# Optimization experiments

Measured on AMD Instinct MI355X. Metric: run time of the kernel, lower is better.

Reference implementation:

```python
import jax, jax.numpy as jnp
import numpy as np

N_NODES = 100000
N_EDGES = 1600000
D_FEAT = 32
D_HID = 64
D_OUT = 64


def setup_inputs() -> dict:
    key = jax.random.key(0)
    ks = jax.random.split(key, 7)
    x = jax.random.normal(ks[0], (N_NODES, D_FEAT), dtype=jnp.float32)
    pos = jax.random.uniform(ks[1], (N_NODES, 3), dtype=jnp.float32) * 100.0
    # Fixed-size stand-in for radius_graph(pos, 5) output: (2, E) [source; target]
    edge_index = jax.random.randint(ks[2], (2, N_EDGES), 0, N_NODES, dtype=jnp.int64)
    d_in = D_FEAT + 3  # concat(x_j, pos_j - pos_i)
    W1 = jax.random.normal(ks[3], (d_in, D_HID), dtype=jnp.float32) / np.sqrt(d_in)
    b1 = jnp.zeros((D_HID,), dtype=jnp.float32)
    W2 = jax.random.normal(ks[4], (D_HID, D_OUT), dtype=jnp.float32) / np.sqrt(D_HID)
    b2 = jnp.zeros((D_OUT,), dtype=jnp.float32)
    return {"x": x, "pos": pos, "edge_index": edge_index,
            "W1": W1, "b1": b1, "W2": W2, "b2": b2}


def reference(x, pos, edge_index, W1, b1, W2, b2):
    n = x.shape[0]
    # PointNetConv default add_self_loops=True (radius_graph used loop=False)
    loops = jnp.arange(n, dtype=edge_index.dtype)
    src = jnp.concatenate([edge_index[0], loops])  # source j
    dst = jnp.concatenate([edge_index[1], loops])  # target i
    # gather: per-edge message input [E+N, d_feat+3]
    msg_in = jnp.concatenate([x[src], pos[src] - pos[dst]], axis=-1)
    # local_nn MLP
    h = jax.nn.relu(msg_in @ W1 + b1) @ W2 + b2
    # scatter: max-aggregate onto target nodes (PointConv aggr='max')
    out = jax.ops.segment_max(h, dst, num_segments=n)
    return out
```

## Files before the change

### kernel.cpp

```cpp
#include <hip/hip_runtime.h>
#include <math.h>

#define N_NODES 100000
#define N_EDGES 1600000
#define D_FEAT 32
#define D_HID 64
#define D_OUT 64
#define CAP 48
#define NPB 64
#define NBKT 1563
#define B1 256
#define E_PER_B1 6250
#define NB_NODE 1024

typedef _Float16 half8 __attribute__((ext_vector_type(8)));
typedef float f32x4  __attribute__((ext_vector_type(4)));

__device__ inline unsigned pk_subrelu(unsigned v, unsigned nq) {
    unsigned r;
    asm("v_pk_add_f16 %0, %1, %2\n\t"
        "v_pk_max_f16 %0, %0, 0"
        : "=v"(r) : "v"(v), "v"(nq));
    return r;
}

__global__ __launch_bounds__(256)
void node_kernel(const float* __restrict__ x,
                 const float* __restrict__ pos,
                 const float* __restrict__ W1,
                 const float* __restrict__ b1,
                 unsigned short* __restrict__ vb,
                 unsigned short* __restrict__ qb) {
    const int lane = threadIdx.x & 63;
    const int wid  = (blockIdx.x * blockDim.x + threadIdx.x) >> 6;
    const int nw   = (NB_NODE * 256) >> 6;

    float w[D_FEAT + 3];
#pragma unroll
    for (int f = 0; f < D_FEAT + 3; ++f)
        w[f] = W1[f * D_HID + lane];
    const float bb = b1[lane];

    for (int node = wid; node < N_NODES; node += nw) {
        const float* xr = x + (size_t)node * D_FEAT;
        float acc = bb;
#pragma unroll
        for (int f = 0; f < D_FEAT; ++f)
            acc = fmaf(xr[f], w[f], acc);

        const float* pr = pos + (size_t)node * 3;
        float qa = 0.0f;
#pragma unroll
        for (int p = 0; p < 3; ++p)
            qa = fmaf(pr[p], w[D_FEAT + p], qa);

        vb[(size_t)node * D_HID + lane] =
            __builtin_bit_cast(unsigned short, (_Float16)(acc + qa));
        qb[(size_t)node * D_HID + lane] =
            __builtin_bit_cast(unsigned short, (_Float16)(-qa));
    }
}

__global__ __launch_bounds__(1024)
void sort_kernel(const int* __restrict__ src,
                 const int* __restrict__ dst,
                 unsigned int* __restrict__ coarse,
                 int* __restrict__ dir) {
    __shared__ int hist[NBKT];
    __shared__ int stage[E_PER_B1];
    __shared__ int wsum[16];

    const int tid  = threadIdx.x;
    const int lane = tid & 63;
    const int wv   = tid >> 6;
    const int e0   = blockIdx.x * E_PER_B1;

    for (int b = tid; b < NBKT; b += 1024) hist[b] = 0;
    __syncthreads();

    for (int e = e0 + tid; e < e0 + E_PER_B1; e += 1024)
        atomicAdd(&hist[dst[e] >> 6], 1);
    __syncthreads();

    const int i0 = tid * 2;
    int c0 = (i0     < NBKT) ? hist[i0]     : 0;
    int c1 = (i0 + 1 < NBKT) ? hist[i0 + 1] : 0;
    const int sum = c0 + c1;
    int inc = sum;
#pragma unroll
    for (int d = 1; d < 64; d <<= 1) {
        int u = __shfl_up(inc, d, 64);
        if (lane >= d) inc += u;
    }
    if (lane == 63) wsum[wv] = inc;
    __syncthreads();
    if (wv == 0) {
        int s = (lane < 16) ? wsum[lane] : 0;
#pragma unroll
        for (int d = 1; d < 16; d <<= 1) {
            int u = __shfl_up(s, d, 64);
            if (lane >= d) s += u;
        }
        if (lane < 16) wsum[lane] = s;
    }
    __syncthreads();
    const int excl = inc - sum + ((wv > 0) ? wsum[wv - 1] : 0);
    if (i0     < NBKT) hist[i0]     = excl;
    if (i0 + 1 < NBKT) hist[i0 + 1] = excl + c0;
    __syncthreads();

    for (int b = tid; b < NBKT; b += 1024)
        dir[(size_t)blockIdx.x * NBKT + b] = e0 + hist[b];
    __syncthreads();

    for (int e = e0 + tid; e < e0 + E_PER_B1; e += 1024) {
        int d = dst[e], s = src[e];
        int p = atomicAdd(&hist[d >> 6], 1);
        stage[p] = (int)(((unsigned)s << 6) | (unsigned)(d & 63));
    }
    __syncthreads();

    for (int i = tid; i < E_PER_B1; i += 1024)
        coarse[e0 + i] = (unsigned)stage[i];
}

__global__ __launch_bounds__(256)
void agg_kernel(const unsigned short* __restrict__ vb,
                const unsigned short* __restrict__ qb,
                const float* __restrict__ W2,
                const float* __restrict__ b2,
                const int* __restrict__ dir,
                const unsigned int* __restrict__ coarse,
                float* __restrict__ out) {
    __shared__ int lcnt[NPB];
    __shared__ int lslots[NPB][CAP];

    const int tid  = threadIdx.x;
    const int lane = tid & 63;
    const int wave = tid >> 6;
    const int quad = lane >> 4;
    const int mrow = lane & 15;
    const int bkt  = blockIdx.x;
    const int nbase = bkt << 6;

    half8 bfrag[4][2];
#pragma unroll
    for (int t = 0; t < 4; ++t)
#pragma unroll
        for (int kh = 0; kh < 2; ++kh) {
            half8 f;
#pragma unroll
            for (int j = 0; j < 8; ++j)
                f[j] = (_Float16)W2[(kh * 32 + quad * 8 + j) * D_OUT + t * 16 + mrow];
            bfrag[t][kh] = f;
        }
    float bias[4];
#pragma unroll
    for (int t = 0; t < 4; ++t) bias[t] = b2[t * 16 + mrow];

    for (int i = tid; i < NPB; i += 256) lcnt[i] = 0;
    __syncthreads();
    {
        const int s0 = dir[(size_t)tid * NBKT + bkt];
        const int s1 = (bkt + 1 < NBKT) ? dir[(size_t)tid * NBKT + bkt + 1]
                                        : (tid + 1) * E_PER_B1;
        for (int j = s0; j < s1; ++j) {
            unsigned enc = coarse[j];
            int local = (int)(enc & 63u);
            int s     = (int)(enc >> 6);
            int p = atomicAdd(&lcnt[local], 1);
            if (p < CAP) lslots[local][p] = s;
        }
    }
    __syncthreads();

    for (int ln = wave; ln < NPB; ln += 4) {
        const int node = nbase + ln;
        if (node >= N_NODES) break;

        const uint4 nq0 = *(const uint4*)(qb + (size_t)node * D_HID + quad * 8);
        const uint4 nq1 = *(const uint4*)(qb + (size_t)node * D_HID + 32 + quad * 8);

        int deg = lcnt[ln];
        if (deg > CAP) deg = CAP;
        const int rows = deg + 1;
        const int nbat = (rows + 15) >> 4;

        float rmax[4][4];
#pragma unroll
        for (int t = 0; t < 4; ++t)
#pragma unroll
            for (int r = 0; r < 4; ++r) rmax[t][r] = -INFINITY;

        for (int b = 0; b < nbat; ++b) {
            int idx = b * 16 + mrow;
            int idxc = (idx < CAP) ? idx : (CAP - 1);
            int s = (idx < deg) ? lslots[ln][idxc] : node;

            const uint4 v0 = *(const uint4*)(vb + (size_t)s * D_HID + quad * 8);
            const uint4 v1 = *(const uint4*)(vb + (size_t)s * D_HID + 32 + quad * 8);

            uint4 a0u, a1u;
            a0u.x = pk_subrelu(v0.x, nq0.x);
            a0u.y = pk_subrelu(v0.y, nq0.y);
            a0u.z = pk_subrelu(v0.z, nq0.z);
            a0u.w = pk_subrelu(v0.w, nq0.w);
            a1u.x = pk_subrelu(v1.x, nq1.x);
            a1u.y = pk_subrelu(v1.y, nq1.y);
            a1u.z = pk_subrelu(v1.z, nq1.z);
            a1u.w = pk_subrelu(v1.w, nq1.w);
            half8 a0 = __builtin_bit_cast(half8, a0u);
            half8 a1 = __builtin_bit_cast(half8, a1u);

#pragma unroll
            for (int t = 0; t < 4; ++t) {
                f32x4 acc = (f32x4){0.f, 0.f, 0.f, 0.f};
                acc = __builtin_amdgcn_mfma_f32_16x16x32_f16(a0, bfrag[t][0], acc, 0, 0, 0);
                acc = __builtin_amdgcn_mfma_f32_16x16x32_f16(a1, bfrag[t][1], acc, 0, 0, 0);
#pragma unroll
                for (int r = 0; r < 4; ++r)
                    rmax[t][r] = fmaxf(rmax[t][r], acc[r]);
            }
        }

        float fin[4];
#pragma unroll
        for (int t = 0; t < 4; ++t) {
            float m = fmaxf(fmaxf(rmax[t][0], rmax[t][1]), fmaxf(rmax[t][2], rmax[t][3]));
            m = fmaxf(m, __shfl_xor(m, 16, 64));
            m = fmaxf(m, __shfl_xor(m, 32, 64));
            fin[t] = m + bias[t];
        }
        float r = (quad == 0) ? fin[0] : (quad == 1) ? fin[1] : (quad == 2) ? fin[2] : fin[3];
        out[(size_t)node * D_OUT + lane] = r;
    }
}

extern "C" void kernel_launch(void* const* d_in, const int* in_sizes, int n_in,
                              void* d_out, int out_size, void* d_ws, size_t ws_size,
                              hipStream_t stream) {
    const float* x   = (const float*)d_in[0];
    const float* pos = (const float*)d_in[1];
    const int*   ei  = (const int*)d_in[2];
    const float* W1  = (const float*)d_in[3];
    const float* b1  = (const float*)d_in[4];
    const float* W2  = (const float*)d_in[5];
    const float* b2  = (const float*)d_in[6];
    float* out = (float*)d_out;

    char* ws = (char*)d_ws;
    unsigned short* vb   = (unsigned short*)ws;
    unsigned short* qb   = (unsigned short*)(ws + 12800000);
    unsigned int* coarse = (unsigned int*)(ws + 25600000);
    int*            dir  = (int*)(ws + 32000000);

    const int* src = ei;
    const int* dst = ei + N_EDGES;

    hipLaunchKernelGGL(sort_kernel, dim3(B1), dim3(1024), 0, stream,
                       src, dst, coarse, dir);
    hipLaunchKernelGGL(node_kernel, dim3(NB_NODE), dim3(256), 0, stream,
                       x, pos, W1, b1, vb, qb);
    hipLaunchKernelGGL(agg_kernel, dim3(NBKT), dim3(256), 0, stream,
                       vb, qb, W2, b2, dir, coarse, out);
}
```

Before: 194.1 us.

## Halve nodes per aggregation bucket and transpose bucket directory layout

Buckets shrink from 64 to 32 destination nodes, doubling the number of aggregation blocks to spread work across more CUs. The sort kernel scans four histogram entries per thread to cover the larger bucket count. The per-block bucket offsets are now stored bucket-major, so each aggregation block reads its 256 start offsets contiguously instead of with a large stride. Each block keeps four waves but now handles only 32 nodes, so per-block setup such as the W2 fragment load is amortised over fewer nodes. The node-bound check is dropped because 3125*32 equals the node count exactly.

```diff
diff --git a/kernel.cpp b/kernel.cpp
--- a/kernel.cpp
+++ b/kernel.cpp
@@ -7,8 +7,8 @@
 #define D_HID 64
 #define D_OUT 64
 #define CAP 48
-#define NPB 64
-#define NBKT 1563
+#define NPB 32
+#define NBKT 3125
 #define B1 256
 #define E_PER_B1 6250
 #define NB_NODE 1024
@@ -65,7 +65,7 @@
 void sort_kernel(const int* __restrict__ src,
                  const int* __restrict__ dst,
                  unsigned int* __restrict__ coarse,
-                 int* __restrict__ dir) {
+                 int* __restrict__ dirT) {
     __shared__ int hist[NBKT];
     __shared__ int stage[E_PER_B1];
     __shared__ int wsum[16];
@@ -79,13 +79,17 @@
     __syncthreads();
 
     for (int e = e0 + tid; e < e0 + E_PER_B1; e += 1024)
-        atomicAdd(&hist[dst[e] >> 6], 1);
-    __syncthreads();
-
-    const int i0 = tid * 2;
-    int c0 = (i0     < NBKT) ? hist[i0]     : 0;
-    int c1 = (i0 + 1 < NBKT) ? hist[i0 + 1] : 0;
-    const int sum = c0 + c1;
+        atomicAdd(&hist[dst[e] >> 5], 1);
+    __syncthreads();
+
+    const int i0 = tid * 4;
+    int c[4];
+    int sum = 0;
+#pragma unroll
+    for (int k = 0; k < 4; ++k) {
+        c[k] = (i0 + k < NBKT) ? hist[i0 + k] : 0;
+        sum += c[k];
+    }
     int inc = sum;
 #pragma unroll
     for (int d = 1; d < 64; d <<= 1) {
@@ -104,19 +108,22 @@
         if (lane < 16) wsum[lane] = s;
     }
     __syncthreads();
-    const int excl = inc - sum + ((wv > 0) ? wsum[wv - 1] : 0);
-    if (i0     < NBKT) hist[i0]     = excl;
-    if (i0 + 1 < NBKT) hist[i0 + 1] = excl + c0;
+    int excl = inc - sum + ((wv > 0) ? wsum[wv - 1] : 0);
+#pragma unroll
+    for (int k = 0; k < 4; ++k) {
+        if (i0 + k < NBKT) hist[i0 + k] = excl;
+        excl += c[k];
+    }
     __syncthreads();
 
     for (int b = tid; b < NBKT; b += 1024)
-        dir[(size_t)blockIdx.x * NBKT + b] = e0 + hist[b];
+        dirT[(size_t)b * B1 + blockIdx.x] = e0 + hist[b];
     __syncthreads();
 
     for (int e = e0 + tid; e < e0 + E_PER_B1; e += 1024) {
         int d = dst[e], s = src[e];
-        int p = atomicAdd(&hist[d >> 6], 1);
-        stage[p] = (int)(((unsigned)s << 6) | (unsigned)(d & 63));
+        int p = atomicAdd(&hist[d >> 5], 1);
+        stage[p] = (int)(((unsigned)s << 5) | (unsigned)(d & 31));
     }
     __syncthreads();
 
@@ -129,7 +136,7 @@
                 const unsigned short* __restrict__ qb,
                 const float* __restrict__ W2,
                 const float* __restrict__ b2,
-                const int* __restrict__ dir,
+                const int* __restrict__ dirT,
                 const unsigned int* __restrict__ coarse,
                 float* __restrict__ out) {
     __shared__ int lcnt[NPB];
@@ -141,7 +148,7 @@
     const int quad = lane >> 4;
     const int mrow = lane & 15;
     const int bkt  = blockIdx.x;
-    const int nbase = bkt << 6;
+    const int nbase = bkt << 5;
 
     half8 bfrag[4][2];
 #pragma unroll
@@ -161,13 +168,13 @@
     for (int i = tid; i < NPB; i += 256) lcnt[i] = 0;
     __syncthreads();
     {
-        const int s0 = dir[(size_t)tid * NBKT + bkt];
-        const int s1 = (bkt + 1 < NBKT) ? dir[(size_t)tid * NBKT + bkt + 1]
+        const int s0 = dirT[(size_t)bkt * B1 + tid];
+        const int s1 = (bkt + 1 < NBKT) ? dirT[(size_t)(bkt + 1) * B1 + tid]
                                         : (tid + 1) * E_PER_B1;
         for (int j = s0; j < s1; ++j) {
             unsigned enc = coarse[j];
-            int local = (int)(enc & 63u);
-            int s     = (int)(enc >> 6);
+            int local = (int)(enc & 31u);
+            int s     = (int)(enc >> 5);
             int p = atomicAdd(&lcnt[local], 1);
             if (p < CAP) lslots[local][p] = s;
         }
@@ -176,7 +183,6 @@
 
     for (int ln = wave; ln < NPB; ln += 4) {
         const int node = nbase + ln;
-        if (node >= N_NODES) break;
 
         const uint4 nq0 = *(const uint4*)(qb + (size_t)node * D_HID + quad * 8);
         const uint4 nq1 = *(const uint4*)(qb + (size_t)node * D_HID + 32 + quad * 8);
@@ -252,15 +258,15 @@
     unsigned short* vb   = (unsigned short*)ws;
     unsigned short* qb   = (unsigned short*)(ws + 12800000);
     unsigned int* coarse = (unsigned int*)(ws + 25600000);
-    int*            dir  = (int*)(ws + 32000000);
+    int*            dirT = (int*)(ws + 32000000);
 
     const int* src = ei;
     const int* dst = ei + N_EDGES;
 
     hipLaunchKernelGGL(sort_kernel, dim3(B1), dim3(1024), 0, stream,
-                       src, dst, coarse, dir);
+                       src, dst, coarse, dirT);
     hipLaunchKernelGGL(node_kernel, dim3(NB_NODE), dim3(256), 0, stream,
                        x, pos, W1, b1, vb, qb);
     hipLaunchKernelGGL(agg_kernel, dim3(NBKT), dim3(256), 0, stream,
-                       vb, qb, W2, b2, dir, coarse, out);
-}
+                       vb, qb, W2, b2, dirT, coarse, out);
+}
```

Result: slower. 199.6 us (+2.8%).
